# Optimization experiments

Measured on AMD Instinct MI355X. Metric: run time of the kernel, lower is better.

The kernel has to match this reference:

```python
import jax, jax.numpy as jnp
import numpy as np

EPS = 1e-7  # K.epsilon()

def setup_inputs() -> dict:
    key = jax.random.key(0)
    k1, k2, k3 = jax.random.split(key, 3)
    B, T, D = 32, 2048, 512
    x = jax.random.normal(k1, (B, T, D), dtype=jnp.float32)
    W = jax.random.normal(k2, (D, D), dtype=jnp.float32) * (1.0 / np.sqrt(D))
    b = jnp.zeros((D,), dtype=jnp.float32)
    u = jax.random.normal(k3, (D,), dtype=jnp.float32) * (1.0 / np.sqrt(D))
    return {"x": x, "W": W, "b": b, "u": u}

def reference(x, W, b, u):
    # uit = tanh(x @ W + b)  -> [B, T, D]
    uit = jnp.tanh(jnp.einsum('btd,de->bte', x, W) + b)
    # scores: sum over feature dim of uit * u -> [B, T]
    ait = jnp.einsum('btd,d->bt', uit, u)
    # exp + normalize over T (no mask); matches original exp/sum form
    a = jnp.exp(ait)
    a = a / (jnp.sum(a, axis=1, keepdims=True) + EPS)
    # weighted sum pooling over T -> [B, D]
    return jnp.einsum('btd,bt->bd', x, a)
```

## Files before the change

kernel.cpp:

```cpp
#include <hip/hip_runtime.h>
#include <math.h>

#define D_DIM 512

typedef short short8v __attribute__((ext_vector_type(8)));
typedef unsigned short ushort8v __attribute__((ext_vector_type(8)));
typedef float f32x16 __attribute__((ext_vector_type(16)));

__device__ inline unsigned short f2bf(float f) {
    union { float f; unsigned int u; } a; a.f = f;
    unsigned int u = a.u;
    unsigned int r = (u + 0x7fffu + ((u >> 16) & 1u)) >> 16;
    return (unsigned short)r;
}

__device__ inline float fast_tanh(float y) {
    float e2 = __expf(2.f * y);
    return 1.f - __fdividef(2.f, e2 + 1.f);
}

#define ASYNC_CP16(gp, lp) \
    __builtin_amdgcn_global_load_lds( \
        (const __attribute__((address_space(1))) void*)(gp), \
        (__attribute__((address_space(3))) void*)(lp), 16, 0, 0)

__global__ __launch_bounds__(1024) void wt_kernel(const float* __restrict__ W,
                                                  unsigned short* __restrict__ Wb2) {
    __shared__ __align__(16) unsigned short lbuf[16384];
    const int s = blockIdx.x;
    const int tid = threadIdx.x;
    #pragma unroll
    for (int i = 0; i < 4; ++i) {
        int flat = tid + i * 1024;
        int kr = flat >> 7;
        int e4 = (flat & 127) * 4;
        float4 v = *(const float4*)(W + (size_t)(s * 32 + kr) * D_DIM + e4);
        int ks = kr >> 4, half = (kr >> 3) & 1, j = kr & 7;
        float vv[4] = {v.x, v.y, v.z, v.w};
        #pragma unroll
        for (int q = 0; q < 4; ++q) {
            int e = e4 + q, nt = e >> 5, nl = e & 31;
            lbuf[(((nt * 2 + ks) * 2 + half) * 32 + nl) * 8 + j] = f2bf(vv[q]);
        }
    }
    __syncthreads();
    #pragma unroll
    for (int i = 0; i < 2; ++i) {
        int c = tid + i * 1024;
        *(ushort8v*)(Wb2 + (size_t)s * 16384 + c * 8) = *(const ushort8v*)&lbuf[c * 8];
    }
}

constexpr int XLDE = 40;

__global__ __launch_bounds__(512, 2) void gemm_ait_mfma(
    const float* __restrict__ x, const unsigned short* __restrict__ Wb2,
    const float* __restrict__ bias, const float* __restrict__ u,
    float* __restrict__ ait)
{
    __shared__ __align__(16) unsigned short wsh[2][16384];
    __shared__ __align__(16) unsigned short xs[2][128 * XLDE];
    __shared__ float rowpart[4][128];

    const int tid  = threadIdx.x;
    const int wave = tid >> 6;
    const int lane = tid & 63;
    const int half = lane >> 5;
    const int nl   = lane & 31;
    const int wr   = wave >> 2;
    const int wc   = wave & 3;
    const int m0   = blockIdx.x * 128;

    f32x16 acc[2][4];
    #pragma unroll
    for (int mi = 0; mi < 2; ++mi)
        #pragma unroll
        for (int ni = 0; ni < 4; ++ni)
            #pragma unroll
            for (int r = 0; r < 16; ++r) acc[mi][ni][r] = 0.f;

    const int xr = tid >> 2;
    const int xc = tid & 3;
    const float* xbase = x + (size_t)(m0 + xr) * D_DIM + xc * 8;

    #pragma unroll
    for (int i = 0; i < 4; ++i)
        ASYNC_CP16(Wb2 + tid * 8 + i * 4096, &wsh[0][tid * 8 + i * 4096]);
    float4 px0 = *(const float4*)(xbase);
    float4 px1 = *(const float4*)(xbase + 4);

    for (int s = 0; s < 16; ++s) {
        const int pb = s & 1;
        {
            ushort8v pk;
            pk[0] = f2bf(px0.x); pk[1] = f2bf(px0.y); pk[2] = f2bf(px0.z); pk[3] = f2bf(px0.w);
            pk[4] = f2bf(px1.x); pk[5] = f2bf(px1.y); pk[6] = f2bf(px1.z); pk[7] = f2bf(px1.w);
            *(ushort8v*)&xs[pb][xr * XLDE + xc * 8] = pk;
        }
        __syncthreads();

        if (s + 1 < 16) {
            const unsigned short* wsrc = Wb2 + (size_t)(s + 1) * 16384;
            #pragma unroll
            for (int i = 0; i < 4; ++i)
                ASYNC_CP16(wsrc + tid * 8 + i * 4096, &wsh[1 - pb][tid * 8 + i * 4096]);
            px0 = *(const float4*)(xbase + (s + 1) * 32);
            px1 = *(const float4*)(xbase + (s + 1) * 32 + 4);
        }

        #pragma unroll
        for (int ks = 0; ks < 2; ++ks) {
            short8v af[2], bfr[4];
            #pragma unroll
            for (int mi = 0; mi < 2; ++mi)
                af[mi] = *(const short8v*)&xs[pb][(wr * 64 + mi * 32 + nl) * XLDE + ks * 16 + half * 8];
            #pragma unroll
            for (int ni = 0; ni < 4; ++ni)
                bfr[ni] = *(const short8v*)&wsh[pb][(((wc * 4 + ni) * 2 + ks) * 2 + half) * 256 + nl * 8];
            #pragma unroll
            for (int mi = 0; mi < 2; ++mi)
                #pragma unroll
                for (int ni = 0; ni < 4; ++ni)
                    acc[mi][ni] = __builtin_amdgcn_mfma_f32_32x32x16_bf16(
                        af[mi], bfr[ni], acc[mi][ni], 0, 0, 0);
        }
    }

    float rowsum[2][16];
    #pragma unroll
    for (int mi = 0; mi < 2; ++mi)
        #pragma unroll
        for (int r = 0; r < 16; ++r) rowsum[mi][r] = 0.f;

    #pragma unroll
    for (int mi = 0; mi < 2; ++mi) {
        #pragma unroll
        for (int ni = 0; ni < 4; ++ni) {
            int col = wc * 128 + ni * 32 + nl;
            float be = bias[col], ue = u[col];
            #pragma unroll
            for (int r = 0; r < 16; ++r)
                rowsum[mi][r] += fast_tanh(acc[mi][ni][r] + be) * ue;
        }
    }
    #pragma unroll
    for (int mi = 0; mi < 2; ++mi)
        #pragma unroll
        for (int r = 0; r < 16; ++r) {
            float v = rowsum[mi][r];
            v += __shfl_xor(v, 1, 64);
            v += __shfl_xor(v, 2, 64);
            v += __shfl_xor(v, 4, 64);
            v += __shfl_xor(v, 8, 64);
            v += __shfl_xor(v, 16, 64);
            rowsum[mi][r] = v;
        }
    if (nl == 0) {
        #pragma unroll
        for (int mi = 0; mi < 2; ++mi)
            #pragma unroll
            for (int r = 0; r < 16; ++r) {
                int row = wr * 64 + mi * 32 + (r & 3) + 8 * (r >> 2) + 4 * half;
                rowpart[wc][row] = rowsum[mi][r];
            }
    }
    __syncthreads();
    if (tid < 128)
        ait[m0 + tid] = rowpart[0][tid] + rowpart[1][tid] + rowpart[2][tid] + rowpart[3][tid];
}

__global__ __launch_bounds__(256) void gemm_ait_f32(
    const float* __restrict__ x, const float* __restrict__ W,
    const float* __restrict__ bias, const float* __restrict__ u,
    float* __restrict__ ait)
{
    __shared__ float xsf[64][68];
    __shared__ float wshf[64][132];
    const int tid = threadIdx.x;
    const int tx = tid & 15, ty = tid >> 4;
    const int m0 = blockIdx.x * 64;
    float rowsum[4] = {0.f, 0.f, 0.f, 0.f};
    for (int e0 = 0; e0 < D_DIM; e0 += 128) {
        float acc[4][8];
        #pragma unroll
        for (int i = 0; i < 4; ++i)
            #pragma unroll
            for (int j = 0; j < 8; ++j) acc[i][j] = 0.f;
        for (int kc = 0; kc < D_DIM; kc += 64) {
            #pragma unroll
            for (int i = 0; i < 4; ++i) {
                int idx = tid + i * 256;
                int r = idx >> 4, c = (idx & 15) * 4;
                *(float4*)&xsf[r][c] = *(const float4*)(x + (size_t)(m0 + r) * D_DIM + kc + c);
            }
            #pragma unroll
            for (int i = 0; i < 8; ++i) {
                int idx = tid + i * 256;
                int r = idx >> 5, c = (idx & 31) * 4;
                *(float4*)&wshf[r][c] = *(const float4*)(W + (size_t)(kc + r) * D_DIM + e0 + c);
            }
            __syncthreads();
            #pragma unroll 4
            for (int k = 0; k < 64; ++k) {
                float xv[4];
                #pragma unroll
                for (int i = 0; i < 4; ++i) xv[i] = xsf[ty * 4 + i][k];
                float4 w0 = *(const float4*)&wshf[k][tx * 8];
                float4 w1 = *(const float4*)&wshf[k][tx * 8 + 4];
                #pragma unroll
                for (int i = 0; i < 4; ++i) {
                    acc[i][0] += xv[i] * w0.x; acc[i][1] += xv[i] * w0.y;
                    acc[i][2] += xv[i] * w0.z; acc[i][3] += xv[i] * w0.w;
                    acc[i][4] += xv[i] * w1.x; acc[i][5] += xv[i] * w1.y;
                    acc[i][6] += xv[i] * w1.z; acc[i][7] += xv[i] * w1.w;
                }
            }
            __syncthreads();
        }
        #pragma unroll
        for (int j = 0; j < 8; ++j) {
            int e = e0 + tx * 8 + j;
            float be = bias[e], ue = u[e];
            #pragma unroll
            for (int i = 0; i < 4; ++i) rowsum[i] += tanhf(acc[i][j] + be) * ue;
        }
    }
    float* red = &xsf[0][0];
    #pragma unroll
    for (int i = 0; i < 4; ++i) red[(ty * 4 + i) * 16 + tx] = rowsum[i];
    __syncthreads();
    if (tid < 64) {
        float s = 0.f;
        #pragma unroll
        for (int j = 0; j < 16; ++j) s += red[tid * 16 + j];
        ait[m0 + tid] = s;
    }
}

__global__ __launch_bounds__(256) void softmax_kernel(float* __restrict__ ait, int T)
{
    const int b = blockIdx.x;
    float* p = ait + (size_t)b * T;
    const int tid = threadIdx.x;
    float ev[8];
    float local = 0.f;
    #pragma unroll
    for (int i = 0; i < 8; ++i) {
        ev[i] = expf(p[tid + i * 256]);
        local += ev[i];
    }
    #pragma unroll
    for (int off = 32; off > 0; off >>= 1)
        local += __shfl_down(local, off, 64);
    __shared__ float wsum[4];
    const int wv = tid >> 6, lane = tid & 63;
    if (lane == 0) wsum[wv] = local;
    __syncthreads();
    float total = wsum[0] + wsum[1] + wsum[2] + wsum[3];
    float inv = 1.0f / (total + 1e-7f);
    #pragma unroll
    for (int i = 0; i < 8; ++i) p[tid + i * 256] = ev[i] * inv;
}

__global__ __launch_bounds__(256) void pool_partial_kernel(
    const float* __restrict__ x, const float* __restrict__ a,
    float* __restrict__ partial, int T)
{
    const int chunks = T >> 8;
    const int b = blockIdx.x / chunks;
    const int c = blockIdx.x % chunks;
    const int tid = threadIdx.x;
    const int th = tid >> 7;
    const int d = (tid & 127) * 4;

    const float* xp = x + ((size_t)b * T + c * 256) * D_DIM + d;
    const float* ap = a + (size_t)b * T + c * 256;

    float4 acc = {0.f, 0.f, 0.f, 0.f};
    #pragma unroll 8
    for (int t = th; t < 256; t += 2) {
        float s = ap[t];
        float4 xv = *(const float4*)(xp + (size_t)t * D_DIM);
        acc.x += xv.x * s; acc.y += xv.y * s;
        acc.z += xv.z * s; acc.w += xv.w * s;
    }
    __shared__ float4 tmp[128];
    if (th == 1) tmp[tid & 127] = acc;
    __syncthreads();
    if (th == 0) {
        float4 o = tmp[tid];
        acc.x += o.x; acc.y += o.y; acc.z += o.z; acc.w += o.w;
        *(float4*)(partial + (size_t)blockIdx.x * D_DIM + tid * 4) = acc;
    }
}

__global__ __launch_bounds__(256) void pool_reduce_kernel(
    const float* __restrict__ partial, float* __restrict__ out, int chunks)
{
    const int b = blockIdx.x;
    const int tid = threadIdx.x;
    const int d = tid * 2;
    float2 acc = {0.f, 0.f};
    for (int c = 0; c < chunks; ++c) {
        float2 v = *(const float2*)(partial + ((size_t)b * chunks + c) * D_DIM + d);
        acc.x += v.x; acc.y += v.y;
    }
    *(float2*)(out + (size_t)b * D_DIM + d) = acc;
}

__global__ __launch_bounds__(256) void pool_atomic_kernel(
    const float* __restrict__ x, const float* __restrict__ a,
    float* __restrict__ out, int T)
{
    const int chunks = T >> 8;
    const int b = blockIdx.x / chunks;
    const int c = blockIdx.x % chunks;
    const int tid = threadIdx.x;
    const int th = tid >> 7;
    const int d = (tid & 127) * 4;
    const float* xp = x + ((size_t)b * T + c * 256) * D_DIM + d;
    const float* ap = a + (size_t)b * T + c * 256;
    float4 acc = {0.f, 0.f, 0.f, 0.f};
    #pragma unroll 8
    for (int t = th; t < 256; t += 2) {
        float s = ap[t];
        float4 xv = *(const float4*)(xp + (size_t)t * D_DIM);
        acc.x += xv.x * s; acc.y += xv.y * s;
        acc.z += xv.z * s; acc.w += xv.w * s;
    }
    __shared__ float4 tmp[128];
    if (th == 1) tmp[tid & 127] = acc;
    __syncthreads();
    if (th == 0) {
        float4 o = tmp[tid];
        float* op = out + (size_t)b * D_DIM + tid * 4;
        atomicAdd(op + 0, acc.x + o.x);
        atomicAdd(op + 1, acc.y + o.y);
        atomicAdd(op + 2, acc.z + o.z);
        atomicAdd(op + 3, acc.w + o.w);
    }
}

extern "C" void kernel_launch(void* const* d_in, const int* in_sizes, int n_in,
                              void* d_out, int out_size, void* d_ws, size_t ws_size,
                              hipStream_t stream)
{
    const float* x    = (const float*)d_in[0];
    const float* W    = (const float*)d_in[1];
    const float* bias = (const float*)d_in[2];
    const float* u    = (const float*)d_in[3];
    float* out = (float*)d_out;

    const int Dd = in_sizes[2];
    const int M  = in_sizes[0] / Dd;
    const int B  = out_size / Dd;
    const int T  = M / B;
    const int chunks = T >> 8;

    const size_t wb_bytes  = (size_t)Dd * Dd * sizeof(unsigned short);
    const size_t ait_bytes = (size_t)M * sizeof(float);

    if (ws_size >= wb_bytes + ait_bytes) {
        unsigned short* Wb2 = (unsigned short*)d_ws;
        float* ait     = (float*)((char*)d_ws + wb_bytes);
        float* partial = (float*)d_ws;

        wt_kernel<<<dim3(16), dim3(1024), 0, stream>>>(W, Wb2);
        gemm_ait_mfma<<<dim3(M / 128), dim3(512), 0, stream>>>(x, Wb2, bias, u, ait);
        softmax_kernel<<<dim3(B), dim3(256), 0, stream>>>(ait, T);
        pool_partial_kernel<<<dim3(B * chunks), dim3(256), 0, stream>>>(x, ait, partial, T);
        pool_reduce_kernel<<<dim3(B), dim3(256), 0, stream>>>(partial, out, chunks);
    } else {
        float* ait = (float*)d_ws;
        gemm_ait_f32<<<dim3(M / 64), dim3(256), 0, stream>>>(x, W, bias, u, ait);
        softmax_kernel<<<dim3(B), dim3(256), 0, stream>>>(ait, T);
        hipMemsetAsync(d_out, 0, (size_t)out_size * sizeof(float), stream);
        pool_atomic_kernel<<<dim3(B * chunks), dim3(256), 0, stream>>>(x, ait, out, T);
    }
}
```

Before: 260.1 us.

## Keep W column slices in registers and stream x directly into MFMA operands

Restructures the bf16 MFMA GEMM so each wave holds a 32-column slice of the bf16 W entirely in registers for the whole K dimension. x rows are loaded straight from global memory with register prefetch and converted in-register using a packed rounding perm, instead of being staged through LDS. Columns are split across two blocks whose partial scores are written to separate buffers and summed in the softmax kernel. The goal is to remove LDS traffic, per-step barriers, and redundant W reloads per tile. The cost is high register pressure (32 short8 operands per lane) and each x row being read by two blocks from global memory; the bf16 rounding also changes from round-to-nearest-even to round-half-up.

Result: slower. 448.9 us (+72.6%).

```diff
diff --git a/kernel.cpp b/kernel.cpp
--- a/kernel.cpp
+++ b/kernel.cpp
@@ -4,7 +4,6 @@
 #define D_DIM 512
 
 typedef short short8v __attribute__((ext_vector_type(8)));
-typedef unsigned short ushort8v __attribute__((ext_vector_type(8)));
 typedef float f32x16 __attribute__((ext_vector_type(16)));
 
 __device__ inline unsigned short f2bf(float f) {
@@ -14,159 +13,148 @@
     return (unsigned short)r;
 }
 
+__device__ inline unsigned int pk2bf(float lo, float hi) {
+    union { float f; unsigned int u; } A, B;
+    A.f = lo; B.f = hi;
+    return __builtin_amdgcn_perm(B.u + 0x8000u, A.u + 0x8000u, 0x07060302u);
+}
+
+__device__ inline short8v cvt8(float4 a, float4 b) {
+    union { unsigned int i[4]; short8v s; } o;
+    o.i[0] = pk2bf(a.x, a.y);
+    o.i[1] = pk2bf(a.z, a.w);
+    o.i[2] = pk2bf(b.x, b.y);
+    o.i[3] = pk2bf(b.z, b.w);
+    return o.s;
+}
+
 __device__ inline float fast_tanh(float y) {
     float e2 = __expf(2.f * y);
     return 1.f - __fdividef(2.f, e2 + 1.f);
 }
 
-#define ASYNC_CP16(gp, lp) \
-    __builtin_amdgcn_global_load_lds( \
-        (const __attribute__((address_space(1))) void*)(gp), \
-        (__attribute__((address_space(3))) void*)(lp), 16, 0, 0)
-
-__global__ __launch_bounds__(1024) void wt_kernel(const float* __restrict__ W,
-                                                  unsigned short* __restrict__ Wb2) {
+__global__ __launch_bounds__(256) void wt_kernel(const float* __restrict__ W,
+                                                 unsigned short* __restrict__ Wb2) {
     __shared__ __align__(16) unsigned short lbuf[16384];
-    const int s = blockIdx.x;
-    const int tid = threadIdx.x;
-    #pragma unroll
-    for (int i = 0; i < 4; ++i) {
-        int flat = tid + i * 1024;
-        int kr = flat >> 7;
-        int e4 = (flat & 127) * 4;
-        float4 v = *(const float4*)(W + (size_t)(s * 32 + kr) * D_DIM + e4);
-        int ks = kr >> 4, half = (kr >> 3) & 1, j = kr & 7;
-        float vv[4] = {v.x, v.y, v.z, v.w};
-        #pragma unroll
-        for (int q = 0; q < 4; ++q) {
-            int e = e4 + q, nt = e >> 5, nl = e & 31;
-            lbuf[(((nt * 2 + ks) * 2 + half) * 32 + nl) * 8 + j] = f2bf(vv[q]);
-        }
-    }
-    __syncthreads();
+    const int ct = blockIdx.x;
+    const int tid = threadIdx.x;
     #pragma unroll
     for (int i = 0; i < 2; ++i) {
-        int c = tid + i * 1024;
-        *(ushort8v*)(Wb2 + (size_t)s * 16384 + c * 8) = *(const ushort8v*)&lbuf[c * 8];
-    }
-}
-
-constexpr int XLDE = 40;
+        int k = tid * 2 + i;
+        const float* wr = W + (size_t)k * D_DIM + ct * 32;
+        int kk = (k >> 4) * 2 + ((k >> 3) & 1);
+        int kj = k & 7;
+        #pragma unroll
+        for (int q = 0; q < 8; ++q) {
+            float4 v = *(const float4*)(wr + q * 4);
+            int e0 = q * 4;
+            lbuf[(kk * 32 + e0 + 0) * 8 + kj] = f2bf(v.x);
+            lbuf[(kk * 32 + e0 + 1) * 8 + kj] = f2bf(v.y);
+            lbuf[(kk * 32 + e0 + 2) * 8 + kj] = f2bf(v.z);
+            lbuf[(kk * 32 + e0 + 3) * 8 + kj] = f2bf(v.w);
+        }
+    }
+    __syncthreads();
+    #pragma unroll
+    for (int i = 0; i < 8; ++i) {
+        int c = tid + i * 256;
+        *(short8v*)(Wb2 + (size_t)ct * 16384 + c * 8) = *(const short8v*)&lbuf[c * 8];
+    }
+}
 
 __global__ __launch_bounds__(512, 2) void gemm_ait_mfma(
     const float* __restrict__ x, const unsigned short* __restrict__ Wb2,
     const float* __restrict__ bias, const float* __restrict__ u,
-    float* __restrict__ ait)
-{
-    __shared__ __align__(16) unsigned short wsh[2][16384];
-    __shared__ __align__(16) unsigned short xs[2][128 * XLDE];
-    __shared__ float rowpart[4][128];
+    float* __restrict__ ait2, int Mtot, int mtiles)
+{
+    __shared__ float rowpart[8][64];
 
     const int tid  = threadIdx.x;
     const int wave = tid >> 6;
     const int lane = tid & 63;
     const int half = lane >> 5;
     const int nl   = lane & 31;
-    const int wr   = wave >> 2;
-    const int wc   = wave & 3;
-    const int m0   = blockIdx.x * 128;
-
-    f32x16 acc[2][4];
-    #pragma unroll
-    for (int mi = 0; mi < 2; ++mi)
-        #pragma unroll
-        for (int ni = 0; ni < 4; ++ni)
-            #pragma unroll
-            for (int r = 0; r < 16; ++r) acc[mi][ni][r] = 0.f;
-
-    const int xr = tid >> 2;
-    const int xc = tid & 3;
-    const float* xbase = x + (size_t)(m0 + xr) * D_DIM + xc * 8;
-
-    #pragma unroll
-    for (int i = 0; i < 4; ++i)
-        ASYNC_CP16(Wb2 + tid * 8 + i * 4096, &wsh[0][tid * 8 + i * 4096]);
-    float4 px0 = *(const float4*)(xbase);
-    float4 px1 = *(const float4*)(xbase + 4);
-
-    for (int s = 0; s < 16; ++s) {
-        const int pb = s & 1;
-        {
-            ushort8v pk;
-            pk[0] = f2bf(px0.x); pk[1] = f2bf(px0.y); pk[2] = f2bf(px0.z); pk[3] = f2bf(px0.w);
-            pk[4] = f2bf(px1.x); pk[5] = f2bf(px1.y); pk[6] = f2bf(px1.z); pk[7] = f2bf(px1.w);
-            *(ushort8v*)&xs[pb][xr * XLDE + xc * 8] = pk;
+    const int ch   = blockIdx.x & 1;
+    const int mg   = blockIdx.x >> 1;
+    const int ct   = ch * 8 + wave;
+    const int col  = ct * 32 + nl;
+
+    short8v breg[32];
+    {
+        const unsigned short* wp = Wb2 + (size_t)ct * 16384 + (half * 32 + nl) * 8;
+        #pragma unroll
+        for (int ks = 0; ks < 32; ++ks)
+            breg[ks] = *(const short8v*)(wp + ks * 512);
+    }
+    const float be = bias[col];
+    const float ue = u[col];
+
+    for (int i = 0; i < mtiles; ++i) {
+        const int m0 = (mg * mtiles + i) * 64;
+        const float* xr0 = x + (size_t)(m0 + nl) * D_DIM + half * 8;
+        const float* xr1 = xr0 + (size_t)32 * D_DIM;
+
+        f32x16 acc0, acc1;
+        #pragma unroll
+        for (int r = 0; r < 16; ++r) { acc0[r] = 0.f; acc1[r] = 0.f; }
+
+        float4 a0[2][2], a1[2][2];
+        #pragma unroll
+        for (int s = 0; s < 2; ++s) {
+            a0[s][0] = *(const float4*)(xr0 + s * 16);
+            a0[s][1] = *(const float4*)(xr0 + s * 16 + 4);
+            a1[s][0] = *(const float4*)(xr1 + s * 16);
+            a1[s][1] = *(const float4*)(xr1 + s * 16 + 4);
+        }
+
+        #pragma unroll
+        for (int ks = 0; ks < 32; ++ks) {
+            const int sl = ks & 1;
+            short8v af0 = cvt8(a0[sl][0], a0[sl][1]);
+            short8v af1 = cvt8(a1[sl][0], a1[sl][1]);
+            if (ks + 2 < 32) {
+                a0[sl][0] = *(const float4*)(xr0 + (ks + 2) * 16);
+                a0[sl][1] = *(const float4*)(xr0 + (ks + 2) * 16 + 4);
+                a1[sl][0] = *(const float4*)(xr1 + (ks + 2) * 16);
+                a1[sl][1] = *(const float4*)(xr1 + (ks + 2) * 16 + 4);
+            }
+            acc0 = __builtin_amdgcn_mfma_f32_32x32x16_bf16(af0, breg[ks], acc0, 0, 0, 0);
+            acc1 = __builtin_amdgcn_mfma_f32_32x32x16_bf16(af1, breg[ks], acc1, 0, 0, 0);
+        }
+
+        float rs0[16], rs1[16];
+        #pragma unroll
+        for (int r = 0; r < 16; ++r) {
+            rs0[r] = fast_tanh(acc0[r] + be) * ue;
+            rs1[r] = fast_tanh(acc1[r] + be) * ue;
+        }
+        #pragma unroll
+        for (int r = 0; r < 16; ++r) {
+            float v0 = rs0[r], v1 = rs1[r];
+            v0 += __shfl_xor(v0, 1, 64);  v1 += __shfl_xor(v1, 1, 64);
+            v0 += __shfl_xor(v0, 2, 64);  v1 += __shfl_xor(v1, 2, 64);
+            v0 += __shfl_xor(v0, 4, 64);  v1 += __shfl_xor(v1, 4, 64);
+            v0 += __shfl_xor(v0, 8, 64);  v1 += __shfl_xor(v1, 8, 64);
+            v0 += __shfl_xor(v0, 16, 64); v1 += __shfl_xor(v1, 16, 64);
+            rs0[r] = v0; rs1[r] = v1;
+        }
+        if (nl == 0) {
+            #pragma unroll
+            for (int r = 0; r < 16; ++r) {
+                int row = (r & 3) + 8 * (r >> 2) + 4 * half;
+                rowpart[wave][row]      = rs0[r];
+                rowpart[wave][row + 32] = rs1[r];
+            }
         }
         __syncthreads();
-
-        if (s + 1 < 16) {
-            const unsigned short* wsrc = Wb2 + (size_t)(s + 1) * 16384;
-            #pragma unroll
-            for (int i = 0; i < 4; ++i)
-                ASYNC_CP16(wsrc + tid * 8 + i * 4096, &wsh[1 - pb][tid * 8 + i * 4096]);
-            px0 = *(const float4*)(xbase + (s + 1) * 32);
-            px1 = *(const float4*)(xbase + (s + 1) * 32 + 4);
-        }
-
-        #pragma unroll
-        for (int ks = 0; ks < 2; ++ks) {
-            short8v af[2], bfr[4];
-            #pragma unroll
-            for (int mi = 0; mi < 2; ++mi)
-                af[mi] = *(const short8v*)&xs[pb][(wr * 64 + mi * 32 + nl) * XLDE + ks * 16 + half * 8];
-            #pragma unroll
-            for (int ni = 0; ni < 4; ++ni)
-                bfr[ni] = *(const short8v*)&wsh[pb][(((wc * 4 + ni) * 2 + ks) * 2 + half) * 256 + nl * 8];
-            #pragma unroll
-            for (int mi = 0; mi < 2; ++mi)
-                #pragma unroll
-                for (int ni = 0; ni < 4; ++ni)
-                    acc[mi][ni] = __builtin_amdgcn_mfma_f32_32x32x16_bf16(
-                        af[mi], bfr[ni], acc[mi][ni], 0, 0, 0);
-        }
-    }
-
-    float rowsum[2][16];
-    #pragma unroll
-    for (int mi = 0; mi < 2; ++mi)
-        #pragma unroll
-        for (int r = 0; r < 16; ++r) rowsum[mi][r] = 0.f;
-
-    #pragma unroll
-    for (int mi = 0; mi < 2; ++mi) {
-        #pragma unroll
-        for (int ni = 0; ni < 4; ++ni) {
-            int col = wc * 128 + ni * 32 + nl;
-            float be = bias[col], ue = u[col];
-            #pragma unroll
-            for (int r = 0; r < 16; ++r)
-                rowsum[mi][r] += fast_tanh(acc[mi][ni][r] + be) * ue;
-        }
-    }
-    #pragma unroll
-    for (int mi = 0; mi < 2; ++mi)
-        #pragma unroll
-        for (int r = 0; r < 16; ++r) {
-            float v = rowsum[mi][r];
-            v += __shfl_xor(v, 1, 64);
-            v += __shfl_xor(v, 2, 64);
-            v += __shfl_xor(v, 4, 64);
-            v += __shfl_xor(v, 8, 64);
-            v += __shfl_xor(v, 16, 64);
-            rowsum[mi][r] = v;
-        }
-    if (nl == 0) {
-        #pragma unroll
-        for (int mi = 0; mi < 2; ++mi)
-            #pragma unroll
-            for (int r = 0; r < 16; ++r) {
-                int row = wr * 64 + mi * 32 + (r & 3) + 8 * (r >> 2) + 4 * half;
-                rowpart[wc][row] = rowsum[mi][r];
-            }
-    }
-    __syncthreads();
-    if (tid < 128)
-        ait[m0 + tid] = rowpart[0][tid] + rowpart[1][tid] + rowpart[2][tid] + rowpart[3][tid];
+        if (tid < 64) {
+            float s = 0.f;
+            #pragma unroll
+            for (int w = 0; w < 8; ++w) s += rowpart[w][tid];
+            ait2[(size_t)ch * Mtot + m0 + tid] = s;
+        }
+        __syncthreads();
+    }
 }
 
 __global__ __launch_bounds__(256) void gemm_ait_f32(
@@ -237,16 +225,21 @@
     }
 }
 
-__global__ __launch_bounds__(256) void softmax_kernel(float* __restrict__ ait, int T)
+__global__ __launch_bounds__(256) void softmax_kernel(float* __restrict__ p,
+                                                      int Mtot, int T, int dual)
 {
     const int b = blockIdx.x;
-    float* p = ait + (size_t)b * T;
+    float* base = p + (size_t)b * T;
+    const float* base2 = p + (size_t)Mtot + (size_t)b * T;
     const int tid = threadIdx.x;
     float ev[8];
     float local = 0.f;
     #pragma unroll
     for (int i = 0; i < 8; ++i) {
-        ev[i] = expf(p[tid + i * 256]);
+        int idx = tid + i * 256;
+        float v = base[idx];
+        if (dual) v += base2[idx];
+        ev[i] = expf(v);
         local += ev[i];
     }
     #pragma unroll
@@ -259,7 +252,7 @@
     float total = wsum[0] + wsum[1] + wsum[2] + wsum[3];
     float inv = 1.0f / (total + 1e-7f);
     #pragma unroll
-    for (int i = 0; i < 8; ++i) p[tid + i * 256] = ev[i] * inv;
+    for (int i = 0; i < 8; ++i) base[tid + i * 256] = ev[i] * inv;
 }
 
 __global__ __launch_bounds__(256) void pool_partial_kernel(
@@ -357,23 +350,26 @@
     const int T  = M / B;
     const int chunks = T >> 8;
 
-    const size_t wb_bytes  = (size_t)Dd * Dd * sizeof(unsigned short);
-    const size_t ait_bytes = (size_t)M * sizeof(float);
-
-    if (ws_size >= wb_bytes + ait_bytes) {
+    const size_t wb_bytes   = (size_t)Dd * Dd * sizeof(unsigned short);
+    const size_t ait2_bytes = 2 * (size_t)M * sizeof(float);
+
+    if (ws_size >= wb_bytes + ait2_bytes) {
         unsigned short* Wb2 = (unsigned short*)d_ws;
-        float* ait     = (float*)((char*)d_ws + wb_bytes);
+        float* ait2    = (float*)((char*)d_ws + wb_bytes);
         float* partial = (float*)d_ws;
 
-        wt_kernel<<<dim3(16), dim3(1024), 0, stream>>>(W, Wb2);
-        gemm_ait_mfma<<<dim3(M / 128), dim3(512), 0, stream>>>(x, Wb2, bias, u, ait);
-        softmax_kernel<<<dim3(B), dim3(256), 0, stream>>>(ait, T);
-        pool_partial_kernel<<<dim3(B * chunks), dim3(256), 0, stream>>>(x, ait, partial, T);
+        const int mtiles = 8;
+        const int grid = 2 * (M / (64 * mtiles));
+
+        wt_kernel<<<dim3(16), dim3(256), 0, stream>>>(W, Wb2);
+        gemm_ait_mfma<<<dim3(grid), dim3(512), 0, stream>>>(x, Wb2, bias, u, ait2, M, mtiles);
+        softmax_kernel<<<dim3(B), dim3(256), 0, stream>>>(ait2, M, T, 1);
+        pool_partial_kernel<<<dim3(B * chunks), dim3(256), 0, stream>>>(x, ait2, partial, T);
         pool_reduce_kernel<<<dim3(B), dim3(256), 0, stream>>>(partial, out, chunks);
     } else {
         float* ait = (float*)d_ws;
         gemm_ait_f32<<<dim3(M / 64), dim3(256), 0, stream>>>(x, W, bias, u, ait);
-        softmax_kernel<<<dim3(B), dim3(256), 0, stream>>>(ait, T);
+        softmax_kernel<<<dim3(B), dim3(256), 0, stream>>>(ait, M, T, 0);
         hipMemsetAsync(d_out, 0, (size_t)out_size * sizeof(float), stream);
         pool_atomic_kernel<<<dim3(B * chunks), dim3(256), 0, stream>>>(x, ait, out, T);
     }
```
